# Optimization experiments

Measured on AMD Instinct MI355X. Metric: run time of the kernel, lower is better.

## Reference

```python
import jax, jax.numpy as jnp
import numpy as np

QK_C = 64
VX_C = 128

def conv1x1(x, W, b):
    # x: [B,C,H,W], W: [O,C], b: [O] -> [B,O,H,W]
    return jnp.einsum('bchw,oc->bohw', x, W) + b[None, :, None, None]

def setup_inputs() -> dict:
    key = jax.random.key(0)
    ks = jax.random.split(key, 9)
    B, H, W = 4, 64, 64
    x = jax.random.normal(ks[0], (B, QK_C, H, W), dtype=jnp.float32)
    x_h = jax.random.normal(ks[1], (B, VX_C, H, W), dtype=jnp.float32)
    qc = QK_C // 4
    s_qk = 1.0 / np.sqrt(QK_C)
    s_v = 1.0 / np.sqrt(VX_C)
    Wq = jax.random.normal(ks[2], (qc, QK_C), dtype=jnp.float32) * s_qk
    bq = jax.random.normal(ks[3], (qc,), dtype=jnp.float32) * 0.01
    Wk = jax.random.normal(ks[4], (qc, QK_C), dtype=jnp.float32) * s_qk
    bk = jax.random.normal(ks[5], (qc,), dtype=jnp.float32) * 0.01
    Wv = jax.random.normal(ks[6], (VX_C, VX_C), dtype=jnp.float32) * s_v
    bv = jax.random.normal(ks[7], (VX_C,), dtype=jnp.float32) * 0.01
    # gamma initialized to zero in the torch module; use a small nonzero value
    # so the attention branch actually contributes to the output/gradients.
    gamma = jnp.array([0.1], dtype=jnp.float32)
    return {"x": x, "x_h": x_h, "Wq": Wq, "bq": bq, "Wk": Wk, "bk": bk,
            "Wv": Wv, "bv": bv, "gamma": gamma}

def reference(x, x_h, Wq, bq, Wk, bk, Wv, bv, gamma):
    B, C, H, W = x_h.shape
    b, c, h, w = x.shape
    N = h * w
    # 1x1-conv projections, flattened over spatial positions
    q = conv1x1(x, Wq, bq).reshape(b, -1, N)          # [B, qc, N]
    k = conv1x1(x, Wk, bk).reshape(b, -1, N)          # [B, qc, N]
    v = conv1x1(x_h, Wv, bv).reshape(B, C, H * W)     # [B, C, N]
    # energy[b, i, j] = <q[:, i], k[:, j]>
    energy = jnp.einsum('bdi,bdj->bij', q, k)          # [B, N, N]
    attention = jax.nn.softmax(energy, axis=-1)
    # out[b, c, i] = sum_j v[b, c, j] * attention[b, i, j]
    out = jnp.einsum('bcj,bij->bci', v, attention)     # [B, C, N]
    out = out.reshape(B, C, H, W)
    return gamma[0] * out + x_h
```

## Files before the change

kernel.cpp:

```cpp
#include <hip/hip_runtime.h>

#define BB 4
#define NN 4096
#define CQK 64
#define DQ 16
#define CV 128

typedef __attribute__((ext_vector_type(8))) short bf16x8;
typedef __attribute__((ext_vector_type(4))) float f32x4;
typedef __attribute__((ext_vector_type(16))) float f32x16;
typedef __attribute__((ext_vector_type(8))) unsigned short u16x8;

__device__ __forceinline__ unsigned short f2bf(float f) {
    unsigned int u = __builtin_bit_cast(unsigned int, f);
    u += 0x7FFFu + ((u >> 16) & 1u);
    return (unsigned short)(u >> 16);
}
__device__ __forceinline__ unsigned int pk_trunc(float lo, float hi) {
    unsigned int a = __builtin_bit_cast(unsigned int, lo);
    unsigned int b = __builtin_bit_cast(unsigned int, hi);
    return (a >> 16) | (b & 0xFFFF0000u);
}

__global__ __launch_bounds__(256, 4) void proj(
    const float* __restrict__ x,
    const float* __restrict__ Wq, const float* __restrict__ bq,
    const float* __restrict__ Wk, const float* __restrict__ bk,
    const float* __restrict__ xh,
    const float* __restrict__ Wv, const float* __restrict__ bv,
    unsigned short* __restrict__ qT, unsigned short* __restrict__ kT,
    unsigned short* __restrict__ vB)
{
    __shared__ __align__(16) float smem[8448];
    int tid = threadIdx.x;
    if (blockIdx.x < 512) {
        float* wvT = smem;
        float* xs  = smem + 4224;
        float* bvs = smem + 8320;
        int pt = blockIdx.x >> 1, h = blockIdx.x & 1;
        int i0 = pt * 64;
        int b = i0 >> 12, ib = i0 & 4095;
        int co0 = h * 64;
        if (tid < 64) bvs[tid] = bv[co0 + tid];
        int cog = tid & 31, ig = tid >> 5;
        float acc[8][2];
#pragma unroll
        for (int q = 0; q < 8; q++) { acc[q][0] = 0.f; acc[q][1] = 0.f; }

        for (int ch = 0; ch < 2; ch++) {
            for (int t = tid; t < 4096; t += 256) {
                int c = t & 63, col = t >> 6;
                wvT[c * 66 + col] = Wv[(size_t)(co0 + col) * CV + ch * 64 + c];
            }
            for (int t = tid; t < 4096; t += 256) {
                int il = t & 63, c = t >> 6;
                xs[c * 64 + il] = xh[((size_t)b * CV + ch * 64 + c) * NN + ib + il];
            }
            __syncthreads();
            for (int c = 0; c < 64; c++) {
                float2 w2 = *(const float2*)&wvT[c * 66 + cog * 2];
                float4 xa = *(const float4*)&xs[c * 64 + ig * 8];
                float4 xb = *(const float4*)&xs[c * 64 + ig * 8 + 4];
                float xv[8] = { xa.x, xa.y, xa.z, xa.w, xb.x, xb.y, xb.z, xb.w };
#pragma unroll
                for (int q = 0; q < 8; q++) {
                    acc[q][0] += xv[q] * w2.x;
                    acc[q][1] += xv[q] * w2.y;
                }
            }
            __syncthreads();
        }
        int kt = ib >> 6;
        int chunk = ig >> 2, quad = ig & 3;
#pragma unroll
        for (int cc = 0; cc < 2; cc++) {
            int co = co0 + cog * 2 + cc;
            int n = co >> 4, cl = co & 15;
            float bb = bvs[cog * 2 + cc];
            u16x8 o;
#pragma unroll
            for (int jj = 0; jj < 8; jj++) o[jj] = f2bf(acc[jj][cc] + bb);
            size_t base = ((size_t)(b * 64 + kt)) * 8192
                        + (size_t)(((chunk * 8 + n) * 64 + quad * 16 + cl)) * 8;
            *(u16x8*)(vB + base) = o;
        }
    } else {
        float* wqT = smem;
        float* wkT = smem + 1024;
        float* bqs = smem + 2048;
        float* bks = smem + 2064;
        for (int t = tid; t < 1024; t += 256) {
            int c = t & 63, d = t >> 6;
            wqT[c * 16 + d] = Wq[d * CQK + c];
            wkT[c * 16 + d] = Wk[d * CQK + c];
        }
        if (tid < DQ) { bqs[tid] = bq[tid]; bks[tid] = bk[tid]; }
        __syncthreads();

        int gidx = (blockIdx.x - 512) * 256 + tid;
        int b = gidx >> 12, i = gidx & 4095;
        float qa[DQ], ka[DQ];
#pragma unroll
        for (int d = 0; d < DQ; d++) { qa[d] = bqs[d]; ka[d] = bks[d]; }
        const float* xp = x + (size_t)b * CQK * NN + i;
        for (int c = 0; c < CQK; c++) {
            float xv = xp[(size_t)c * NN];
            const float4* wq4 = (const float4*)&wqT[c * DQ];
            const float4* wk4 = (const float4*)&wkT[c * DQ];
#pragma unroll
            for (int dd = 0; dd < 4; dd++) {
                float4 a = wq4[dd], e = wk4[dd];
                qa[dd*4+0] += a.x * xv; qa[dd*4+1] += a.y * xv;
                qa[dd*4+2] += a.z * xv; qa[dd*4+3] += a.w * xv;
                ka[dd*4+0] += e.x * xv; ka[dd*4+1] += e.y * xv;
                ka[dd*4+2] += e.z * xv; ka[dd*4+3] += e.w * xv;
            }
        }
        u16x8 q0, q1, k0, k1;
#pragma unroll
        for (int dd = 0; dd < 8; dd++) {
            q0[dd] = f2bf(qa[dd]);     q1[dd] = f2bf(qa[8 + dd]);
            k0[dd] = f2bf(ka[dd]);     k1[dd] = f2bf(ka[8 + dd]);
        }
        u16x8* qo = (u16x8*)(qT + (size_t)gidx * DQ);
        u16x8* ko = (u16x8*)(kT + (size_t)gidx * DQ);
        qo[0] = q0; qo[1] = q1;
        ko[0] = k0; ko[1] = k1;
    }
}

__global__ __launch_bounds__(256, 2) void flash_mfma(
    const unsigned short* __restrict__ qTb,
    const unsigned short* __restrict__ kTb,
    const unsigned short* __restrict__ vB,
    const float* __restrict__ xh,
    const float* __restrict__ gamma,
    float* __restrict__ out)
{
    __shared__ __align__(16) unsigned short pT[4 * 32 * 76];
    __shared__ __align__(16) float accs[128 * 36];
    __shared__ float l_s[4 * 2 * 32];

    int tid = threadIdx.x;
    int w = tid >> 6, lane = tid & 63;
    int q32 = lane & 31, half = lane >> 5;
    int quad = lane >> 4, cl = lane & 15;
    int b = blockIdx.x >> 7;
    int i0 = (blockIdx.x & 127) * 32;
    const f32x4 zf = {0.f, 0.f, 0.f, 0.f};
    f32x16 zf16;
#pragma unroll
    for (int r = 0; r < 16; r++) zf16[r] = 0.f;

    bf16x8 qa = *(const bf16x8*)(qTb + ((size_t)(b * NN + i0 + q32)) * DQ + half * 8);

    f32x4 acc[2][8];
#pragma unroll
    for (int g = 0; g < 2; g++)
#pragma unroll
        for (int n = 0; n < 8; n++) acc[g][n] = zf;
    float l = 0.f;

    const unsigned short* vtile = vB + ((size_t)(b * 64 + w * 16)) * 8192;
    const unsigned short* kbase = kTb + ((size_t)(b * NN + w * 16 * 64)) * DQ;
    unsigned short* pTw = pT + w * 32 * 76;

    bf16x8 kb[2], vb[16];
#pragma unroll
    for (int mg = 0; mg < 2; mg++)
        kb[mg] = *(const bf16x8*)(kbase + (size_t)(mg * 32 + q32) * DQ + half * 8);
#pragma unroll
    for (int i = 0; i < 16; i++)
        vb[i] = *(const bf16x8*)(vtile + (size_t)i * 512 + (size_t)lane * 8);

    for (int t = 0; t < 16; t++) {
        f32x16 s[2];
        s[0] = __builtin_amdgcn_mfma_f32_32x32x16_bf16(kb[0], qa, zf16, 0, 0, 0);
        s[1] = __builtin_amdgcn_mfma_f32_32x32x16_bf16(kb[1], qa, zf16, 0, 0, 0);
        const unsigned short* ktn = kbase + (size_t)(((t + 1) & 15) * 64) * DQ;
#pragma unroll
        for (int mg = 0; mg < 2; mg++)
            kb[mg] = *(const bf16x8*)(ktn + (size_t)(mg * 32 + q32) * DQ + half * 8);

#pragma unroll
        for (int mg = 0; mg < 2; mg++) {
#pragma unroll
            for (int rr = 0; rr < 4; rr++) {
                float p0 = __expf(s[mg][rr * 4 + 0]);
                float p1 = __expf(s[mg][rr * 4 + 1]);
                float p2 = __expf(s[mg][rr * 4 + 2]);
                float p3 = __expf(s[mg][rr * 4 + 3]);
                l += (p0 + p1) + (p2 + p3);
                int k0 = mg * 32 + rr * 8 + half * 4;
                *(uint2*)(pTw + q32 * 76 + k0) =
                    make_uint2(pk_trunc(p0, p1), pk_trunc(p2, p3));
            }
        }

        const unsigned short* vtn = vtile + ((t < 15) ? 8192 : 0);
#pragma unroll
        for (int ch = 0; ch < 2; ch++) {
            bf16x8 pa0 = *(const bf16x8*)(pTw + (size_t)cl * 76 + ch * 32 + quad * 8);
            bf16x8 pa1 = *(const bf16x8*)(pTw + (size_t)(16 + cl) * 76 + ch * 32 + quad * 8);
#pragma unroll
            for (int n = 0; n < 8; n++) {
                acc[0][n] = __builtin_amdgcn_mfma_f32_16x16x32_bf16(pa0, vb[ch * 8 + n], acc[0][n], 0, 0, 0);
                acc[1][n] = __builtin_amdgcn_mfma_f32_16x16x32_bf16(pa1, vb[ch * 8 + n], acc[1][n], 0, 0, 0);
            }
#pragma unroll
            for (int n = 0; n < 8; n++)
                vb[ch * 8 + n] = *(const bf16x8*)(vtn + (size_t)(ch * 8 + n) * 512 + (size_t)lane * 8);
        }
        vtile = vtn;
    }

    l_s[(w * 2 + half) * 32 + q32] = l;
    for (int ww = 0; ww < 4; ww++) {
        if (w == ww) {
#pragma unroll
            for (int g = 0; g < 2; g++)
#pragma unroll
                for (int n = 0; n < 8; n++) {
                    float* p = accs + (n * 16 + cl) * 36 + g * 16 + quad * 4;
                    if (ww == 0) *(f32x4*)p = acc[g][n];
                    else {
                        f32x4 o = *(const f32x4*)p;
                        *(f32x4*)p = o + acc[g][n];
                    }
                }
        }
        __syncthreads();
    }

    float gam = gamma[0];
    int q = tid & 31, cg = tid >> 5;
    float L = 0.f;
#pragma unroll
    for (int u = 0; u < 8; u++) L += l_s[u * 32 + q];
    float linv = 1.f / L;
#pragma unroll
    for (int cc = 0; cc < 16; cc++) {
        int c = cg * 16 + cc;
        size_t gi = ((size_t)(b * CV + c)) * NN + i0 + q;
        out[gi] = gam * accs[c * 36 + q] * linv + xh[gi];
    }
}

extern "C" void kernel_launch(void* const* d_in, const int* in_sizes, int n_in,
                              void* d_out, int out_size, void* d_ws, size_t ws_size,
                              hipStream_t stream)
{
    (void)in_sizes; (void)n_in; (void)out_size; (void)ws_size;
    const float* x  = (const float*)d_in[0];
    const float* xh = (const float*)d_in[1];
    const float* Wq = (const float*)d_in[2];
    const float* bq = (const float*)d_in[3];
    const float* Wk = (const float*)d_in[4];
    const float* bk = (const float*)d_in[5];
    const float* Wv = (const float*)d_in[6];
    const float* bv = (const float*)d_in[7];
    const float* gm = (const float*)d_in[8];
    float* out = (float*)d_out;

    char* ws = (char*)d_ws;
    unsigned short* qTb = (unsigned short*)ws;
    unsigned short* kTb = (unsigned short*)(ws + (512 << 10));
    unsigned short* vB  = (unsigned short*)(ws + (1 << 20));

    proj<<<576, 256, 0, stream>>>(x, Wq, bq, Wk, bk, xh, Wv, bv, qTb, kTb, vB);
    flash_mfma<<<BB * 128, 256, 0, stream>>>(qTb, kTb, vB, xh, gm, out);
}
```

Measured before the change: 124.2 us.

## Keep softmax probabilities in registers via permlane32 swap and 32x32 MFMA for PV

The PV product switches from 16x16x32 MFMAs fed by probabilities staged through LDS to 32x32x16 MFMAs. The exponentiated scores now feed the B operand directly after a v_permlane32_swap reshuffle, with no shared-memory round trip for P. The V projection output layout is reordered to match the new operand fragment, and the projection block order is changed so the small q/k blocks come first. The aim is to remove LDS stores and loads and the associated waits in the inner loop, at the cost of relying on gfx950-specific permlane instructions and a new accumulator reduction layout.

```diff
diff --git a/kernel.cpp b/kernel.cpp
--- a/kernel.cpp
+++ b/kernel.cpp
@@ -10,6 +10,7 @@
 typedef __attribute__((ext_vector_type(4))) float f32x4;
 typedef __attribute__((ext_vector_type(16))) float f32x16;
 typedef __attribute__((ext_vector_type(8))) unsigned short u16x8;
+typedef __attribute__((ext_vector_type(4))) unsigned int u32x4;
 
 __device__ __forceinline__ unsigned short f2bf(float f) {
     unsigned int u = __builtin_bit_cast(unsigned int, f);
@@ -33,11 +34,12 @@
 {
     __shared__ __align__(16) float smem[8448];
     int tid = threadIdx.x;
-    if (blockIdx.x < 512) {
+    if (blockIdx.x >= 64) {
         float* wvT = smem;
         float* xs  = smem + 4224;
         float* bvs = smem + 8320;
-        int pt = blockIdx.x >> 1, h = blockIdx.x & 1;
+        int bid = blockIdx.x - 64;
+        int pt = bid >> 1, h = bid & 1;
         int i0 = pt * 64;
         int b = i0 >> 12, ib = i0 & 4095;
         int co0 = h * 64;
@@ -71,17 +73,17 @@
             __syncthreads();
         }
         int kt = ib >> 6;
-        int chunk = ig >> 2, quad = ig & 3;
+        int hb = ig & 1, kc = ig >> 1;
 #pragma unroll
         for (int cc = 0; cc < 2; cc++) {
             int co = co0 + cog * 2 + cc;
-            int n = co >> 4, cl = co & 15;
+            int g = co >> 5, cl = co & 31;
             float bb = bvs[cog * 2 + cc];
             u16x8 o;
 #pragma unroll
             for (int jj = 0; jj < 8; jj++) o[jj] = f2bf(acc[jj][cc] + bb);
             size_t base = ((size_t)(b * 64 + kt)) * 8192
-                        + (size_t)(((chunk * 8 + n) * 64 + quad * 16 + cl)) * 8;
+                        + (size_t)(((g * 4 + kc) * 64 + hb * 32 + cl)) * 8;
             *(u16x8*)(vB + base) = o;
         }
     } else {
@@ -97,7 +99,7 @@
         if (tid < DQ) { bqs[tid] = bq[tid]; bks[tid] = bk[tid]; }
         __syncthreads();
 
-        int gidx = (blockIdx.x - 512) * 256 + tid;
+        int gidx = blockIdx.x * 256 + tid;
         int b = gidx >> 12, i = gidx & 4095;
         float qa[DQ], ka[DQ];
 #pragma unroll
@@ -137,33 +139,27 @@
     const float* __restrict__ gamma,
     float* __restrict__ out)
 {
-    __shared__ __align__(16) unsigned short pT[4 * 32 * 76];
-    __shared__ __align__(16) float accs[128 * 36];
+    __shared__ __align__(16) float accs[32 * 132];
     __shared__ float l_s[4 * 2 * 32];
 
     int tid = threadIdx.x;
     int w = tid >> 6, lane = tid & 63;
     int q32 = lane & 31, half = lane >> 5;
-    int quad = lane >> 4, cl = lane & 15;
     int b = blockIdx.x >> 7;
     int i0 = (blockIdx.x & 127) * 32;
-    const f32x4 zf = {0.f, 0.f, 0.f, 0.f};
     f32x16 zf16;
 #pragma unroll
     for (int r = 0; r < 16; r++) zf16[r] = 0.f;
 
     bf16x8 qa = *(const bf16x8*)(qTb + ((size_t)(b * NN + i0 + q32)) * DQ + half * 8);
 
-    f32x4 acc[2][8];
-#pragma unroll
-    for (int g = 0; g < 2; g++)
-#pragma unroll
-        for (int n = 0; n < 8; n++) acc[g][n] = zf;
+    f32x16 acc[4];
+#pragma unroll
+    for (int g = 0; g < 4; g++) acc[g] = zf16;
     float l = 0.f;
 
     const unsigned short* vtile = vB + ((size_t)(b * 64 + w * 16)) * 8192;
     const unsigned short* kbase = kTb + ((size_t)(b * NN + w * 16 * 64)) * DQ;
-    unsigned short* pTw = pT + w * 32 * 76;
 
     bf16x8 kb[2], vb[16];
 #pragma unroll
@@ -182,34 +178,31 @@
         for (int mg = 0; mg < 2; mg++)
             kb[mg] = *(const bf16x8*)(ktn + (size_t)(mg * 32 + q32) * DQ + half * 8);
 
-#pragma unroll
-        for (int mg = 0; mg < 2; mg++) {
-#pragma unroll
-            for (int rr = 0; rr < 4; rr++) {
-                float p0 = __expf(s[mg][rr * 4 + 0]);
-                float p1 = __expf(s[mg][rr * 4 + 1]);
-                float p2 = __expf(s[mg][rr * 4 + 2]);
-                float p3 = __expf(s[mg][rr * 4 + 3]);
-                l += (p0 + p1) + (p2 + p3);
-                int k0 = mg * 32 + rr * 8 + half * 4;
-                *(uint2*)(pTw + q32 * 76 + k0) =
-                    make_uint2(pk_trunc(p0, p1), pk_trunc(p2, p3));
-            }
-        }
-
         const unsigned short* vtn = vtile + ((t < 15) ? 8192 : 0);
 #pragma unroll
-        for (int ch = 0; ch < 2; ch++) {
-            bf16x8 pa0 = *(const bf16x8*)(pTw + (size_t)cl * 76 + ch * 32 + quad * 8);
-            bf16x8 pa1 = *(const bf16x8*)(pTw + (size_t)(16 + cl) * 76 + ch * 32 + quad * 8);
-#pragma unroll
-            for (int n = 0; n < 8; n++) {
-                acc[0][n] = __builtin_amdgcn_mfma_f32_16x16x32_bf16(pa0, vb[ch * 8 + n], acc[0][n], 0, 0, 0);
-                acc[1][n] = __builtin_amdgcn_mfma_f32_16x16x32_bf16(pa1, vb[ch * 8 + n], acc[1][n], 0, 0, 0);
-            }
-#pragma unroll
-            for (int n = 0; n < 8; n++)
-                vb[ch * 8 + n] = *(const bf16x8*)(vtn + (size_t)(ch * 8 + n) * 512 + (size_t)lane * 8);
+        for (int u = 0; u < 4; u++) {
+            const int mg = u >> 1, h8 = (u & 1) * 8;
+            float p0 = __expf(s[mg][h8 + 0]);
+            float p1 = __expf(s[mg][h8 + 1]);
+            float p2 = __expf(s[mg][h8 + 2]);
+            float p3 = __expf(s[mg][h8 + 3]);
+            float p4 = __expf(s[mg][h8 + 4]);
+            float p5 = __expf(s[mg][h8 + 5]);
+            float p6 = __expf(s[mg][h8 + 6]);
+            float p7 = __expf(s[mg][h8 + 7]);
+            l += ((p0 + p1) + (p2 + p3)) + ((p4 + p5) + (p6 + p7));
+            unsigned int A0 = pk_trunc(p0, p1), A1 = pk_trunc(p2, p3);
+            unsigned int A2 = pk_trunc(p4, p5), A3 = pk_trunc(p6, p7);
+            asm("v_permlane32_swap_b32 %0, %1" : "+v"(A0), "+v"(A2));
+            asm("v_permlane32_swap_b32 %0, %1" : "+v"(A1), "+v"(A3));
+            u32x4 pbw = { A0, A1, A2, A3 };
+            bf16x8 pb = __builtin_bit_cast(bf16x8, pbw);
+#pragma unroll
+            for (int g = 0; g < 4; g++)
+                acc[g] = __builtin_amdgcn_mfma_f32_32x32x16_bf16(vb[g * 4 + u], pb, acc[g], 0, 0, 0);
+#pragma unroll
+            for (int g = 0; g < 4; g++)
+                vb[g * 4 + u] = *(const bf16x8*)(vtn + (size_t)(g * 4 + u) * 512 + (size_t)lane * 8);
         }
         vtile = vtn;
     }
@@ -218,15 +211,13 @@
     for (int ww = 0; ww < 4; ww++) {
         if (w == ww) {
 #pragma unroll
-            for (int g = 0; g < 2; g++)
-#pragma unroll
-                for (int n = 0; n < 8; n++) {
-                    float* p = accs + (n * 16 + cl) * 36 + g * 16 + quad * 4;
-                    if (ww == 0) *(f32x4*)p = acc[g][n];
-                    else {
-                        f32x4 o = *(const f32x4*)p;
-                        *(f32x4*)p = o + acc[g][n];
-                    }
+            for (int g = 0; g < 4; g++)
+#pragma unroll
+                for (int r = 0; r < 4; r++) {
+                    float* p = accs + q32 * 132 + g * 32 + r * 8 + half * 4;
+                    f32x4 v4 = { acc[g][r*4+0], acc[g][r*4+1], acc[g][r*4+2], acc[g][r*4+3] };
+                    if (ww == 0) *(f32x4*)p = v4;
+                    else { f32x4 o = *(const f32x4*)p; *(f32x4*)p = o + v4; }
                 }
         }
         __syncthreads();
@@ -242,7 +233,7 @@
     for (int cc = 0; cc < 16; cc++) {
         int c = cg * 16 + cc;
         size_t gi = ((size_t)(b * CV + c)) * NN + i0 + q;
-        out[gi] = gam * accs[c * 36 + q] * linv + xh[gi];
+        out[gi] = gam * accs[q * 132 + c] * linv + xh[gi];
     }
 }
 
```

Result: faster. 121.3 us (-2.3%).
